# Kernel tuning notes

Measured on AMD Instinct MI355X. Metric: run time of the kernel, lower is better.

The kernel has to match this reference:

```python
import jax, jax.numpy as jnp
import numpy as np

N_NODES = 50000
N_EDGES = 800000
D_IN = 128
D_HID = 128
N_CLS = 40


def setup_inputs() -> dict:
    key = jax.random.key(0)
    ks = jax.random.split(key, 9)
    x = jax.random.normal(ks[0], (N_NODES, D_IN), dtype=jnp.float32)
    edge_index = jax.random.randint(ks[1], (2, N_EDGES), 0, N_NODES, dtype=jnp.int64)
    def lin(k, fan_in, fan_out):
        bound = 1.0 / np.sqrt(fan_in)
        return jax.random.uniform(k, (fan_in, fan_out), jnp.float32, -bound, bound)
    params = {
        'w1_l': lin(ks[2], D_IN, D_HID), 'w1_r': lin(ks[3], D_IN, D_HID),
        'b1': jnp.zeros((D_HID,), jnp.float32),
        'w2_l': lin(ks[4], D_HID, D_HID), 'w2_r': lin(ks[5], D_HID, D_HID),
        'b2': jnp.zeros((D_HID,), jnp.float32),
        'w3_l': lin(ks[6], D_HID, N_CLS), 'w3_r': lin(ks[7], D_HID, N_CLS),
        'b3': jnp.zeros((N_CLS,), jnp.float32),
    }
    return {'x': x, 'edge_index': edge_index, **params}


def _sage_layer(x, src, dst, w_l, w_r, b):
    # mean-aggregate messages from src -> dst, then lin_l(agg) + lin_r(x) + b, relu
    msgs = x[src]                                             # [E, d] gather
    agg = jax.ops.segment_sum(msgs, dst, num_segments=x.shape[0])  # [N, d]
    deg = jax.ops.segment_sum(jnp.ones((src.shape[0],), x.dtype), dst,
                              num_segments=x.shape[0])        # [N]
    agg = agg / jnp.maximum(deg, 1.0)[:, None]
    out = agg @ w_l + x @ w_r + b
    return jax.nn.relu(out)  # dropout p=0.0 -> identity


def reference(x, edge_index, w1_l, w1_r, b1, w2_l, w2_r, b2, w3_l, w3_r, b3):
    src, dst = edge_index[0], edge_index[1]
    h = _sage_layer(x, src, dst, w1_l, w1_r, b1)
    h = _sage_layer(h, src, dst, w2_l, w2_r, b2)
    h = _sage_layer(h, src, dst, w3_l, w3_r, b3)
    return h
```

## Files before the change

kernel.cpp:

```cpp
#include <hip/hip_runtime.h>
#include <hip/hip_bf16.h>

#define NN 50000
#define NE 800000
#define DD 128
#define NCLS 40
#define NBK ((NN + 255) >> 8)
#define EPB 1024
#define PB ((NE + EPB - 1) / EPB)
#define CVB ((NN * DD / 4) / 256)
#define WB 384
#define SEMAX 5120

typedef _Float16 f16x8 __attribute__((ext_vector_type(8)));
typedef _Float16 f16x4 __attribute__((ext_vector_type(4)));
typedef float f32x4 __attribute__((ext_vector_type(4)));

__device__ __forceinline__ unsigned int pack2h(_Float16 a, _Float16 b) {
    union { _Float16 h[2]; unsigned int u; } c;
    c.h[0] = a; c.h[1] = b;
    return c.u;
}
__device__ __forceinline__ void unpack2h(unsigned int p, float& a, float& b) {
    union { unsigned int u; _Float16 h[2]; } c;
    c.u = p;
    a = (float)c.h[0]; b = (float)c.h[1];
}


__global__ void k_front(const int* __restrict__ ei, int* __restrict__ cellcnt,
                        int* __restrict__ celloff, unsigned int* __restrict__ pairs,
                        const float* __restrict__ x, unsigned short* __restrict__ xh,
                        const float* __restrict__ w1l, const float* __restrict__ w1r,
                        const float* __restrict__ w2l, const float* __restrict__ w2r,
                        const float* __restrict__ w3l, const float* __restrict__ w3r,
                        unsigned short* __restrict__ bt1h,
                        unsigned short* __restrict__ bt2h,
                        unsigned short* __restrict__ bt3h) {
    if (blockIdx.x >= PB + CVB) {
        int idx = blockIdx.x - (PB + CVB);
        int w = idx >> 1, half = idx & 1;
        int ks = w & 7, tmp = w >> 3;
        int nt = tmp & 7, layer = tmp >> 3;
        const int NT = (layer == 2) ? 3 : 8;
        const int NC = (layer == 2) ? NCLS : DD;
        if (nt >= NT) return;
        const float* wl = (layer == 0) ? w1l : (layer == 1) ? w2l : w3l;
        const float* wr = (layer == 0) ? w1r : (layer == 1) ? w2r : w3r;
        unsigned short* bh = (layer == 0) ? bt1h : (layer == 1) ? bt2h : bt3h;
        int t = threadIdx.x;
        int j = t & 7, lane = (t >> 3) + half * 32;
        int row = nt * 16 + (lane & 15);
        int k = ks * 32 + (lane >> 4) * 8 + j;
        float v = 0.f;
        if (row < NC)
            v = (k < 128) ? wl[(size_t)k * NC + row] : wr[(size_t)(k - 128) * NC + row];
        union { _Float16 f; unsigned short u; } ch;
        ch.f = (_Float16)v;
        bh[((size_t)(ks * NT + nt) * 64 + lane) * 8 + j] = ch.u;
        return;
    }
    if (blockIdx.x >= PB) {
        int i = (blockIdx.x - PB) * 256 + threadIdx.x;
        float4 v = ((const float4*)x)[i];
        f16x4 h;
        h[0] = (_Float16)v.x; h[1] = (_Float16)v.y;
        h[2] = (_Float16)v.z; h[3] = (_Float16)v.w;
        int row = i >> 5;
        int f = i & 31;
        int plane = f >> 3;
        int pc = (f & 7) * 4;
        *(f16x4*)(xh + ((size_t)plane * NN + row) * 32 + pc) = h;
        return;
    }
    __shared__ int hist[NBK];
    __shared__ int s[256];
    __shared__ unsigned int sE[EPB];
    __shared__ int nz;
    const int t = threadIdx.x, blk = blockIdx.x;
    const int e0 = blk * EPB;
    if (t == 0) nz = 0;
    for (int i = t; i < NBK; i += 256) hist[i] = 0;
    __syncthreads();
    int any = 0;
    for (int i = t; i < EPB; i += 256)
        if (ei[2 * e0 + 2 * i + 1] != 0) any = 1;
    if (any) atomicOr(&nz, 1);
    __syncthreads();
    const int is64 = (nz == 0);
    unsigned int v[EPB / 256];
    int eb[EPB / 256], er[EPB / 256];
#pragma unroll
    for (int j = 0; j < EPB / 256; ++j) {
        int e = e0 + j * 256 + t;
        if (e < NE) {
            int sv, d;
            if (is64) { sv = ei[2 * e]; d = ei[2 * (NE + e)]; }
            else      { sv = ei[e];     d = ei[NE + e]; }
            v[j] = ((unsigned)sv << 16) | (unsigned)d;
            eb[j] = d >> 8;
            er[j] = atomicAdd(&hist[eb[j]], 1);
        } else {
            eb[j] = -1;
        }
    }
    __syncthreads();
    int hv = (t < NBK) ? hist[t] : 0;
    s[t] = hv;
    __syncthreads();
#pragma unroll
    for (int off = 1; off < 256; off <<= 1) {
        int u = (t >= off) ? s[t - off] : 0;
        __syncthreads();
        s[t] += u;
        __syncthreads();
    }
#pragma unroll
    for (int j = 0; j < EPB / 256; ++j)
        if (eb[j] >= 0) sE[s[eb[j]] - hist[eb[j]] + er[j]] = v[j];
    __syncthreads();
    ((uint4*)(pairs + (size_t)blk * EPB))[t] = ((const uint4*)sE)[t];
    for (int i = t; i < NBK; i += 256) {
        cellcnt[(size_t)i * PB + blk] = hist[i];
        celloff[(size_t)i * PB + blk] = s[i] - hist[i];
    }
}

__global__ void k_scan_ba(const int* __restrict__ cellcnt, int* __restrict__ bsum) {
    __shared__ int red[256];
    int b = blockIdx.x, t = threadIdx.x;
    int acc = 0;
    for (int i = t; i < PB; i += 256) acc += cellcnt[(size_t)b * PB + i];
    red[t] = acc;
    __syncthreads();
#pragma unroll
    for (int off = 128; off > 0; off >>= 1) {
        if (t < off) red[t] += red[t + off];
        __syncthreads();
    }
    if (t == 0) bsum[b] = red[0];
}

__global__ void k_fill2(const unsigned int* __restrict__ pairs,
                        const int* __restrict__ cellcnt,
                        const int* __restrict__ celloff,
                        const int* __restrict__ bsum,
                        int* __restrict__ row_ptr, unsigned short* __restrict__ srcs) {
    __shared__ unsigned int sE[SEMAX];
    __shared__ int hist[256];
    __shared__ int cur[256];
    __shared__ int sb[256];
    __shared__ int scnt;
    const int b = blockIdx.x, t = threadIdx.x;
    if (t < 256) {
        int v = (t < NBK) ? bsum[t] : 0;
        sb[t] = v;
    }
    if (t == 0) scnt = 0;
    if (t < 256) hist[t] = 0;
    __syncthreads();
#pragma unroll
    for (int off = 1; off < 256; off <<= 1) {
        int u = (t >= off && t < 256) ? sb[t - off] : 0;
        __syncthreads();
        if (t < 256) sb[t] += u;
        __syncthreads();
    }
    const int bbase = (b == 0) ? 0 : sb[b - 1];
    if (b == NBK - 1 && t == 0) row_ptr[NN] = sb[NBK - 1];
    for (int blk = t; blk < PB; blk += 512) {
        int cnt = cellcnt[(size_t)b * PB + blk];
        if (cnt) {
            int off = celloff[(size_t)b * PB + blk];
            int base = atomicAdd(&scnt, cnt);
            if (base + cnt <= SEMAX) {
                const unsigned int* pp = pairs + (size_t)blk * EPB + off;
                for (int j = 0; j < cnt; ++j) {
                    unsigned int v = pp[j];
                    sE[base + j] = v;
                    atomicAdd(&hist[v & 255u], 1);
                }
            }
        }
    }
    __syncthreads();
    int h = (t < 256) ? hist[t] : 0;
    if (t < 256) cur[t] = h;
    __syncthreads();
#pragma unroll
    for (int off = 1; off < 256; off <<= 1) {
        int u = (t >= off && t < 256) ? cur[t - off] : 0;
        __syncthreads();
        if (t < 256) cur[t] += u;
        __syncthreads();
    }
    if (t < 256) {
        int node = (b << 8) + t;
        int base = bbase + cur[t] - h;
        if (node < NN) row_ptr[node] = base;
        cur[t] = base;
    }
    __syncthreads();
    int total = min(scnt, SEMAX);
    for (int i = t; i < total; i += 512) {
        unsigned int v = sE[i];
        int pos = atomicAdd(&cur[v & 255u], 1);
        srcs[pos] = (unsigned short)(v >> 16);
    }
}

__global__ __launch_bounds__(256, 8)
void k_agg8(const unsigned int* __restrict__ inq, const int* __restrict__ row_ptr,
            const unsigned short* __restrict__ srcs, unsigned int* __restrict__ oq) {
    const int tid = threadIdx.x;
    const int quarter = (blockIdx.x & 7) >> 1;
    const int parity  = blockIdx.x & 1;
    const int node = ((blockIdx.x >> 3) * 2 + parity) * 16 + (tid >> 4);
    const int pc = tid & 15;
    const unsigned int* tab = inq + (size_t)quarter * NN * 16;
    const int vn = node < NN ? node : NN - 1;
    int b = row_ptr[vn], e = row_ptr[vn + 1];
    int deg = (node < NN) ? (e - b) : 0;
    int m = deg;
    m = max(m, __shfl_xor(m, 16));
    m = max(m, __shfl_xor(m, 32));
    float a0 = 0.f, a1 = 0.f;
    for (int base = 0; base < m; base += 16) {
        unsigned int p[16];
#pragma unroll
        for (int j = 0; j < 16; ++j) {
            int idx = b + base + j;
            idx = idx < e ? idx : (e - 1);
            idx = idx < 0 ? 0 : idx;
            idx = min(idx, NE - 1);
            p[j] = tab[(size_t)srcs[idx] * 16 + pc];
        }
#pragma unroll
        for (int j = 0; j < 16; ++j) {
            float u0, u1;
            unpack2h(p[j], u0, u1);
            if (base + j < deg) { a0 += u0; a1 += u1; }
        }
    }
    if (node < NN) {
        float inv = 1.0f / (float)(deg > 0 ? deg : 1);
        oq[((size_t)quarter * NN + node) * 16 + pc] =
            pack2h((_Float16)(a0 * inv), (_Float16)(a1 * inv));
    }
}

template <int NT, int KPS, bool PACKOUT>
__launch_bounds__(256, 4)
__global__ void k_mfma(const unsigned short* __restrict__ A1h,
                       const unsigned short* __restrict__ A2h,
                       const unsigned short* __restrict__ Bthf,
                       const float* __restrict__ bias, float* __restrict__ outf,
                       unsigned short* __restrict__ outh, const int NC) {
    constexpr int STAGE_ELEMS = KPS * NT * 64 * 8;
    constexpr int STAGE_U4 = STAGE_ELEMS / 8;
    __shared__ unsigned short sBh[STAGE_ELEMS];

    const int tid = threadIdx.x;
    const int wave = tid >> 6, lane = tid & 63;
    const int quad = lane >> 4, mr = lane & 15;
    const int m0 = blockIdx.x * 64 + wave * 16;
    const int row = m0 + mr;
    const bool rok = row < NN;

    f32x4 acc[NT] = {};
    const f16x8 zero = {};

    auto aload = [&](int ks) -> f16x8 {
        const unsigned short* base = (ks < 4) ? A1h : A2h;
        const int plane = ks & 3;
        return rok ? *(const f16x8*)(base + ((size_t)plane * NN + row) * 32 + quad * 8)
                   : zero;
    };

    f16x8 cah = aload(0), pah;

#pragma unroll
    for (int s = 0; s < 8 / KPS; ++s) {
        const uint4* gh = (const uint4*)(Bthf + (size_t)s * STAGE_ELEMS);
        uint4* lh = (uint4*)sBh;
        if (s) __syncthreads();
        for (int i = tid; i < STAGE_U4; i += 256) lh[i] = gh[i];
        __syncthreads();

#pragma unroll
        for (int kl = 0; kl < KPS; ++kl) {
            const int ks = s * KPS + kl;
            if (ks < 7) pah = aload(ks + 1);
#pragma unroll
            for (int n = 0; n < NT; ++n) {
                const int fo = ((kl * NT + n) * 64 + lane) * 8;
                f16x8 bh = *(const f16x8*)(sBh + fo);
                acc[n] = __builtin_amdgcn_mfma_f32_16x16x32_f16(cah, bh, acc[n], 0, 0, 0);
            }
            cah = pah;
        }
    }

#pragma unroll
    for (int n = 0; n < NT; ++n) {
        int col = n * 16 + mr;
        float bv = (col < NC) ? bias[col] : 0.f;
#pragma unroll
        for (int r = 0; r < 4; ++r) {
            int orow = m0 + quad * 4 + r;
            if (orow < NN && col < NC) {
                float v = acc[n][r] + bv;
                v = v > 0.f ? v : 0.f;
                if (PACKOUT) {
                    union { _Float16 f; unsigned short u; } ch;
                    ch.f = (_Float16)v;
                    int pl = col >> 5, pcc = col & 31;
                    outh[((size_t)pl * NN + orow) * 32 + pcc] = ch.u;
                } else {
                    outf[(size_t)orow * NC + col] = v;
                }
            }
        }
    }
}

__global__ __launch_bounds__(256, 4)
void k_gemm3(const unsigned short* __restrict__ Ah,
             const unsigned short* __restrict__ Bthf,
             const float* __restrict__ bias,
             unsigned short* __restrict__ zh, float* __restrict__ yf) {
    __shared__ unsigned short sBh[8 * 3 * 64 * 8];
    const int tid = threadIdx.x;
    const int wave = tid >> 6, lane = tid & 63;
    const int quad = lane >> 4, mr = lane & 15;
    const int m0 = blockIdx.x * 64 + wave * 16;
    const int row = m0 + mr;
    const bool rok = row < NN;

    const uint4* gh = (const uint4*)Bthf;
    uint4* lh = (uint4*)sBh;
    for (int i = tid; i < (8 * 3 * 64 * 8) / 8; i += 256) lh[i] = gh[i];

    const f16x8 zero = {};
    f16x8 a[4];
#pragma unroll
    for (int j = 0; j < 4; ++j)
        a[j] = rok ? *(const f16x8*)(Ah + ((size_t)j * NN + row) * 32 + quad * 8)
                   : zero;
    __syncthreads();

    f32x4 accl[3] = {}, accr[3] = {};
#pragma unroll
    for (int ks = 0; ks < 4; ++ks) {
#pragma unroll
        for (int n = 0; n < 3; ++n) {
            f16x8 bl = *(const f16x8*)(sBh + ((ks * 3 + n) * 64 + lane) * 8);
            accl[n] = __builtin_amdgcn_mfma_f32_16x16x32_f16(a[ks], bl, accl[n], 0, 0, 0);
            f16x8 br = *(const f16x8*)(sBh + (((ks + 4) * 3 + n) * 64 + lane) * 8);
            accr[n] = __builtin_amdgcn_mfma_f32_16x16x32_f16(a[ks], br, accr[n], 0, 0, 0);
        }
    }

#pragma unroll
    for (int n = 0; n < 3; ++n) {
        int col = n * 16 + mr;
        float bv = (col < NCLS) ? bias[col] : 0.f;
#pragma unroll
        for (int r = 0; r < 4; ++r) {
            int orow = m0 + quad * 4 + r;
            if (orow < NN) {
                union { _Float16 f; unsigned short u; } ch;
                ch.f = (_Float16)accl[n][r];
                zh[(size_t)orow * 64 + col] = ch.u;
                if (col < NCLS) yf[(size_t)orow * 40 + col] = accr[n][r] + bv;
            }
        }
    }
}

__global__ __launch_bounds__(256, 8)
void k_agg3(const unsigned int* __restrict__ zu,
            const int* __restrict__ row_ptr,
            const unsigned short* __restrict__ srcs,
            const float* __restrict__ yf, float* __restrict__ out) {
    const int tid = threadIdx.x;
    const int wave = tid >> 6, lane = tid & 63;
    const int half = lane >> 5, hl = lane & 31;
    const int node = blockIdx.x * 8 + wave * 2 + half;
    int b = row_ptr[node], e = row_ptr[node + 1];
    int deg = e - b;
    int od = __shfl_xor(deg, 32);
    int md = max(deg, od);
    float a0 = 0.f, a1 = 0.f;
    for (int base = 0; base < md; base += 16) {
        unsigned int p[16];
#pragma unroll
        for (int j = 0; j < 16; ++j) {
            int idx = b + base + j;
            idx = idx < e ? idx : (e - 1);
            idx = idx < 0 ? 0 : idx;
            idx = min(idx, NE - 1);
            p[j] = zu[(size_t)srcs[idx] * 32 + hl];
        }
#pragma unroll
        for (int j = 0; j < 16; ++j) {
            float u0, u1;
            unpack2h(p[j], u0, u1);
            if (base + j < deg) { a0 += u0; a1 += u1; }
        }
    }
    float inv = 1.0f / (float)(deg > 0 ? deg : 1);
    if (hl < 20) {
        float2 yv = ((const float2*)yf)[(size_t)node * 20 + hl];
        float2 o;
        o.x = fmaxf(a0 * inv + yv.x, 0.f);
        o.y = fmaxf(a1 * inv + yv.y, 0.f);
        ((float2*)out)[(size_t)node * 20 + hl] = o;
    }
}

extern "C" void kernel_launch(void* const* d_in, const int* in_sizes, int n_in,
                              void* d_out, int out_size, void* d_ws, size_t ws_size,
                              hipStream_t stream) {
    const float* x    = (const float*)d_in[0];
    const int*   ei   = (const int*)d_in[1];
    const float* w1_l = (const float*)d_in[2];
    const float* w1_r = (const float*)d_in[3];
    const float* b1   = (const float*)d_in[4];
    const float* w2_l = (const float*)d_in[5];
    const float* w2_r = (const float*)d_in[6];
    const float* b2   = (const float*)d_in[7];
    const float* w3_l = (const float*)d_in[8];
    const float* w3_r = (const float*)d_in[9];
    const float* b3   = (const float*)d_in[10];
    float* out = (float*)d_out;

    char* w = (char*)d_ws;
    size_t off = 0;
    auto alloc = [&](size_t bytes) -> void* {
        void* p = w + off;
        off += (bytes + 255) / 256 * 256;
        return p;
    };
    int* row_ptr = (int*)alloc((size_t)(NN + 1) * 4);
    unsigned short* srcs = (unsigned short*)alloc((size_t)NE * 2 + 64);
    int* cellcnt = (int*)alloc((size_t)NBK * PB * 4);
    int* celloff = (int*)alloc((size_t)NBK * PB * 4);
    int* bsum    = (int*)alloc((size_t)NBK * 4);
    unsigned int* pairs = (unsigned int*)alloc((size_t)PB * EPB * 4);
    unsigned short* xh   = (unsigned short*)alloc((size_t)NN * DD * 2);
    unsigned short* aggh = (unsigned short*)alloc((size_t)NN * DD * 2);
    unsigned short* h1h  = (unsigned short*)alloc((size_t)NN * DD * 2);
    unsigned short* zh   = (unsigned short*)alloc((size_t)NN * 64 * 2);
    float*          yf   = (float*)alloc((size_t)NN * 40 * 4);
    unsigned short* bt1h = (unsigned short*)alloc((size_t)8 * 8 * 64 * 8 * 2);
    unsigned short* bt2h = (unsigned short*)alloc((size_t)8 * 8 * 64 * 8 * 2);
    unsigned short* bt3h = (unsigned short*)alloc((size_t)8 * 3 * 64 * 8 * 2);
    unsigned short* h2h = xh;
    (void)ws_size;

    k_front<<<PB + CVB + WB, 256, 0, stream>>>(ei, cellcnt, celloff, pairs, x, xh,
                                               w1_l, w1_r, w2_l, w2_r, w3_l, w3_r,
                                               bt1h, bt2h, bt3h);
    k_scan_ba<<<NBK, 256, 0, stream>>>(cellcnt, bsum);
    k_fill2<<<NBK, 512, 0, stream>>>(pairs, cellcnt, celloff, bsum, row_ptr, srcs);

    const int gmb = (NN + 63) / 64;
    const int gq = 8 * ((NN + 31) / 32);
    k_agg8<<<gq, 256, 0, stream>>>((const unsigned int*)xh, row_ptr, srcs,
                                   (unsigned int*)aggh);
    k_mfma<8, 4, true><<<gmb, 256, 0, stream>>>(aggh, xh, bt1h, b1,
                                                nullptr, h1h, DD);
    k_agg8<<<gq, 256, 0, stream>>>((const unsigned int*)h1h, row_ptr, srcs,
                                   (unsigned int*)aggh);
    k_mfma<8, 4, true><<<gmb, 256, 0, stream>>>(aggh, h1h, bt2h, b2,
                                                nullptr, h2h, DD);
    k_gemm3<<<gmb, 256, 0, stream>>>(h2h, bt3h, b3, zh, yf);
    k_agg3<<<NN / 8, 256, 0, stream>>>((const unsigned int*)zh, row_ptr, srcs,
                                       yf, out);
}
```

Before: 244.7 us.

## Assign one wave per node and split edges across lane groups in aggregation

The aggregation kernels now map one wavefront to each destination node. Lane groups process different edges in parallel, and the partial sums are combined with cross-lane shuffles. Previously several nodes shared a wave and were padded to the largest degree among them. The new mapping is meant to cut the work wasted on that padding and to put more gather loads in flight per node. In exchange it launches more blocks, adds shuffle reductions, and leaves some lanes idle on the final write.

New measurement: 280.7 us. 14.7% more time.

```diff
diff --git a/kernel.cpp b/kernel.cpp
--- a/kernel.cpp
+++ b/kernel.cpp
@@ -210,41 +210,43 @@
 }
 
 __global__ __launch_bounds__(256, 8)
-void k_agg8(const unsigned int* __restrict__ inq, const int* __restrict__ row_ptr,
+void k_aggp(const unsigned int* __restrict__ inq, const int* __restrict__ row_ptr,
             const unsigned short* __restrict__ srcs, unsigned int* __restrict__ oq) {
     const int tid = threadIdx.x;
-    const int quarter = (blockIdx.x & 7) >> 1;
-    const int parity  = blockIdx.x & 1;
-    const int node = ((blockIdx.x >> 3) * 2 + parity) * 16 + (tid >> 4);
-    const int pc = tid & 15;
-    const unsigned int* tab = inq + (size_t)quarter * NN * 16;
-    const int vn = node < NN ? node : NN - 1;
-    int b = row_ptr[vn], e = row_ptr[vn + 1];
-    int deg = (node < NN) ? (e - b) : 0;
-    int m = deg;
-    m = max(m, __shfl_xor(m, 16));
-    m = max(m, __shfl_xor(m, 32));
+    const int wave = tid >> 6, lane = tid & 63;
+    const int plane = (blockIdx.x & 7) >> 1;
+    const int node = (((blockIdx.x >> 3) << 1) + (blockIdx.x & 1)) * 4 + wave;
+    if (node >= NN) return;
+    const int eg = lane >> 4;
+    const int pc = lane & 15;
+    const unsigned int* tab = inq + (size_t)plane * NN * 16;
+    const int b = row_ptr[node], e = row_ptr[node + 1];
+    const int deg = e - b;
     float a0 = 0.f, a1 = 0.f;
-    for (int base = 0; base < m; base += 16) {
-        unsigned int p[16];
-#pragma unroll
-        for (int j = 0; j < 16; ++j) {
-            int idx = b + base + j;
-            idx = idx < e ? idx : (e - 1);
-            idx = idx < 0 ? 0 : idx;
-            idx = min(idx, NE - 1);
+    for (int base = 0; base < deg; base += 16) {
+        unsigned int p[4];
+        float m[4];
+#pragma unroll
+        for (int j = 0; j < 4; ++j) {
+            int o = base + j * 4 + eg;
+            bool ok = o < deg;
+            m[j] = ok ? 1.f : 0.f;
+            int idx = b + (ok ? o : 0);
             p[j] = tab[(size_t)srcs[idx] * 16 + pc];
         }
 #pragma unroll
-        for (int j = 0; j < 16; ++j) {
+        for (int j = 0; j < 4; ++j) {
             float u0, u1;
             unpack2h(p[j], u0, u1);
-            if (base + j < deg) { a0 += u0; a1 += u1; }
-        }
-    }
-    if (node < NN) {
+            a0 += m[j] * u0;
+            a1 += m[j] * u1;
+        }
+    }
+    a0 += __shfl_xor(a0, 16); a0 += __shfl_xor(a0, 32);
+    a1 += __shfl_xor(a1, 16); a1 += __shfl_xor(a1, 32);
+    if (eg == 0) {
         float inv = 1.0f / (float)(deg > 0 ? deg : 1);
-        oq[((size_t)quarter * NN + node) * 16 + pc] =
+        oq[((size_t)plane * NN + node) * 16 + pc] =
             pack2h((_Float16)(a0 * inv), (_Float16)(a1 * inv));
     }
 }
@@ -385,37 +387,40 @@
             const float* __restrict__ yf, float* __restrict__ out) {
     const int tid = threadIdx.x;
     const int wave = tid >> 6, lane = tid & 63;
-    const int half = lane >> 5, hl = lane & 31;
-    const int node = blockIdx.x * 8 + wave * 2 + half;
-    int b = row_ptr[node], e = row_ptr[node + 1];
-    int deg = e - b;
-    int od = __shfl_xor(deg, 32);
-    int md = max(deg, od);
+    const int eg = lane >> 5;
+    const int c = lane & 31;
+    const int node = blockIdx.x * 4 + wave;
+    const int b = row_ptr[node], e = row_ptr[node + 1];
+    const int deg = e - b;
     float a0 = 0.f, a1 = 0.f;
-    for (int base = 0; base < md; base += 16) {
-        unsigned int p[16];
-#pragma unroll
-        for (int j = 0; j < 16; ++j) {
-            int idx = b + base + j;
-            idx = idx < e ? idx : (e - 1);
-            idx = idx < 0 ? 0 : idx;
-            idx = min(idx, NE - 1);
-            p[j] = zu[(size_t)srcs[idx] * 32 + hl];
-        }
-#pragma unroll
-        for (int j = 0; j < 16; ++j) {
+    for (int base = 0; base < deg; base += 8) {
+        unsigned int p[4];
+        float m[4];
+#pragma unroll
+        for (int j = 0; j < 4; ++j) {
+            int o = base + j * 2 + eg;
+            bool ok = o < deg;
+            m[j] = ok ? 1.f : 0.f;
+            int idx = b + (ok ? o : 0);
+            p[j] = zu[(size_t)srcs[idx] * 32 + c];
+        }
+#pragma unroll
+        for (int j = 0; j < 4; ++j) {
             float u0, u1;
             unpack2h(p[j], u0, u1);
-            if (base + j < deg) { a0 += u0; a1 += u1; }
-        }
-    }
-    float inv = 1.0f / (float)(deg > 0 ? deg : 1);
-    if (hl < 20) {
-        float2 yv = ((const float2*)yf)[(size_t)node * 20 + hl];
+            a0 += m[j] * u0;
+            a1 += m[j] * u1;
+        }
+    }
+    a0 += __shfl_xor(a0, 32);
+    a1 += __shfl_xor(a1, 32);
+    if (eg == 0 && c < 20) {
+        float inv = 1.0f / (float)(deg > 0 ? deg : 1);
+        float2 yv = ((const float2*)yf)[(size_t)node * 20 + c];
         float2 o;
         o.x = fmaxf(a0 * inv + yv.x, 0.f);
         o.y = fmaxf(a1 * inv + yv.y, 0.f);
-        ((float2*)out)[(size_t)node * 20 + hl] = o;
+        ((float2*)out)[(size_t)node * 20 + c] = o;
     }
 }
 
@@ -466,16 +471,16 @@
     k_fill2<<<NBK, 512, 0, stream>>>(pairs, cellcnt, celloff, bsum, row_ptr, srcs);
 
     const int gmb = (NN + 63) / 64;
-    const int gq = 8 * ((NN + 31) / 32);
-    k_agg8<<<gq, 256, 0, stream>>>((const unsigned int*)xh, row_ptr, srcs,
+    const int gp = 8 * ((NN + 7) / 8);
+    k_aggp<<<gp, 256, 0, stream>>>((const unsigned int*)xh, row_ptr, srcs,
                                    (unsigned int*)aggh);
     k_mfma<8, 4, true><<<gmb, 256, 0, stream>>>(aggh, xh, bt1h, b1,
                                                 nullptr, h1h, DD);
-    k_agg8<<<gq, 256, 0, stream>>>((const unsigned int*)h1h, row_ptr, srcs,
+    k_aggp<<<gp, 256, 0, stream>>>((const unsigned int*)h1h, row_ptr, srcs,
                                    (unsigned int*)aggh);
     k_mfma<8, 4, true><<<gmb, 256, 0, stream>>>(aggh, h1h, bt2h, b2,
                                                 nullptr, h2h, DD);
     k_gemm3<<<gmb, 256, 0, stream>>>(h2h, bt3h, b3, zh, yf);
-    k_agg3<<<NN / 8, 256, 0, stream>>>((const unsigned int*)zh, row_ptr, srcs,
+    k_agg3<<<NN / 4, 256, 0, stream>>>((const unsigned int*)zh, row_ptr, srcs,
                                        yf, out);
 }
```
